# Kernel tuning notes

Measured on AMD Instinct MI355X. Metric: run time of the kernel, lower is better.

The kernel has to match this reference:

```python
import jax, jax.numpy as jnp
import numpy as np

LN_EPS = 1e-5

def _layer_norm(z, w, b):
    m = jnp.mean(z, axis=-1, keepdims=True)
    v = jnp.mean(jnp.square(z - m), axis=-1, keepdims=True)
    return (z - m) * jax.lax.rsqrt(v + LN_EPS) * w + b

def setup_inputs() -> dict:
    key = jax.random.key(0)
    ks = jax.random.split(key, 4)
    B, T, H, L = 32, 512, 1024, 2
    scale = 1.0 / np.sqrt(H)
    x = jax.random.normal(ks[0], (B, T, H), dtype=jnp.float32)
    W = jax.random.normal(ks[1], (L, 4 * H, H), dtype=jnp.float32) * scale
    U = jax.random.normal(ks[2], (L, 4 * H, H), dtype=jnp.float32) * scale
    b = jnp.zeros((L, 4 * H), dtype=jnp.float32)
    lng_w = jnp.ones((L, 4 * H), dtype=jnp.float32)
    lng_b = jnp.zeros((L, 4 * H), dtype=jnp.float32)
    lnc_w = jnp.ones((L, H), dtype=jnp.float32)
    lnc_b = jnp.zeros((L, H), dtype=jnp.float32)
    return {"x": x, "W": W, "b": b, "U": U,
            "lng_w": lng_w, "lng_b": lng_b, "lnc_w": lnc_w, "lnc_b": lnc_b}

def reference(x, W, b, U, lng_w, lng_b, lnc_w, lnc_b):
    # x: (B,T,C). Multi-layer MI-LSTM; dropout=0 (eval). Returns y: (B,T,H).
    L = W.shape[0]
    H = lnc_w.shape[1]
    B = x.shape[0]

    def step(carry, xt):
        hs, cs = carry  # each (L,B,H)
        inp = xt        # (B,C)
        new_h, new_c = [], []
        for l in range(L):
            gx = inp @ W[l].T + b[l]          # (B,4H)
            gh = hs[l] @ U[l].T               # (B,4H)
            gates = gx + gh + gx * gh          # multiplicative integration
            gates = _layer_norm(gates, lng_w[l], lng_b[l])
            i, f, g, o = jnp.split(gates, 4, axis=-1)
            c = jax.nn.sigmoid(f) * cs[l] + jax.nn.sigmoid(i) * jnp.tanh(g)
            c = _layer_norm(c, lnc_w[l], lnc_b[l])
            h = jax.nn.sigmoid(o) * jnp.tanh(c)
            inp = h
            new_h.append(h)
            new_c.append(c)
        return (jnp.stack(new_h), jnp.stack(new_c)), inp

    init = (jnp.zeros((L, B, H), x.dtype), jnp.zeros((L, B, H), x.dtype))
    _, ys = jax.lax.scan(step, init, jnp.swapaxes(x, 0, 1))  # ys: (T,B,H)
    return jnp.swapaxes(ys, 0, 1)
```

## Files before the change

### kernel.cpp

```cpp
#include <hip/hip_runtime.h>


#define TSTEPS 512
#define BATCH  32
#define HDIM   1024
#define GDIM   4096
#define NBLK   256
#define NTHR   256
#define CPB    16
#define KPAD   1032

typedef __attribute__((ext_vector_type(8))) short short8;
typedef __attribute__((ext_vector_type(4))) float f32x4;

#define WLO_OFF   0u
#define HPL_OFF   33554432u
#define G_OFF     37748736u
#define SYNC_OFF  39845888u
#define SMEM_BYTES 152640

#define SW_CENSUS(s)  ((s) * 16)
#define SW_FCNT       128
#define SW_SCNT(s)    (144 + (s) * 16)
#define SW_ROOT       272
#define SW_LCNT(s)    (288 + (s) * 16)

#define AT_RLX __ATOMIC_RELAXED
#define SC_AGT __HIP_MEMORY_SCOPE_AGENT

__device__ __forceinline__ unsigned f2bf(float f) {
  unsigned u = __float_as_uint(f);
  return (u + 0x7FFFu + ((u >> 16) & 1u)) >> 16;
}
__device__ __forceinline__ float sigm(float x) { return 1.f / (1.f + __expf(-x)); }
__device__ __forceinline__ float tanh_(float x) { return 1.f - 2.f / (__expf(2.f * x) + 1.f); }

__device__ __forceinline__ void split8(float4 a, float4 b, short8& hi, short8& lo) {
  float f[8] = {a.x, a.y, a.z, a.w, b.x, b.y, b.z, b.w};
  #pragma unroll
  for (int i = 0; i < 8; ++i) {
    unsigned h = f2bf(f[i]);
    hi[i] = (short)h;
    lo[i] = (short)f2bf(f[i] - __uint_as_float(h << 16));
  }
}

__device__ __forceinline__ int xcc_id() {
  return (int)(__builtin_amdgcn_s_getreg(20 | (3 << 11)) & 7);
}

__device__ __forceinline__ unsigned short* hplane(unsigned char* hbase, int slot, int par, int pl) {
  return (unsigned short*)(hbase + ((unsigned)((slot * 8 + par * 4 + pl)) << 16));
}
__device__ __forceinline__ float* gbase(unsigned char* gb, int l, int par) {
  return (float*)(gb + ((unsigned)(l * 2 + par) << 19));
}

__device__ __forceinline__ void gbar(unsigned* sync, int slot, int n, int nslots, unsigned ep) {
  __syncthreads();
  if (threadIdx.x == 0) {
    unsigned a = __hip_atomic_fetch_add(sync + SW_SCNT(slot), 1u, AT_RLX, SC_AGT);
    if (a == (unsigned)n * ep - 1u)
      __hip_atomic_fetch_add(sync + SW_ROOT, 1u, AT_RLX, SC_AGT);
    while (__hip_atomic_load(sync + SW_ROOT, AT_RLX, SC_AGT) < (unsigned)nslots * ep)
      __builtin_amdgcn_s_sleep(4);
  }
  __syncthreads();
  asm volatile("buffer_inv sc0" ::: "memory");
}

__device__ __forceinline__ void lbar(unsigned* sync, int slot, unsigned target) {
  __syncthreads();
  if (threadIdx.x == 0) {
    __hip_atomic_fetch_add(sync + SW_LCNT(slot), 1u, AT_RLX, SC_AGT);
    while (__hip_atomic_load(sync + SW_LCNT(slot), AT_RLX, SC_AGT) < target)
      __builtin_amdgcn_s_sleep(2);
  }
  __syncthreads();
  asm volatile("buffer_inv sc0" ::: "memory");
}

__device__ __forceinline__ void bred(float& s, float& q, volatile float* red, int tid) {
  #pragma unroll
  for (int o = 32; o > 0; o >>= 1) {
    s += __shfl_xor(s, o, 64);
    q += __shfl_xor(q, o, 64);
  }
  __syncthreads();
  if ((tid & 63) == 0) { int w = tid >> 6; red[w] = s; red[w + 4] = q; }
  __syncthreads();
  s = red[0] + red[1] + red[2] + red[3];
  q = red[4] + red[5] + red[6] + red[7];
  __syncthreads();
}

__device__ __forceinline__ void pointwise2(
    int l, int r, int t, const float* __restrict__ gbuf,
    const float* __restrict__ lngw, const float* __restrict__ lngb,
    const float* __restrict__ lncw, const float* __restrict__ lncb,
    unsigned short* __restrict__ hhi, unsigned short* __restrict__ hlo,
    float* __restrict__ y, float* cst, volatile float* red, int tid)
{
  const float* grow = gbuf + (size_t)r * GDIM;
  const int j0 = tid * 4;
  const float* p0 = grow + j0;
  const float* p1 = grow + 1024 + j0;
  const float* p2 = grow + 2048 + j0;
  const float* p3 = grow + 3072 + j0;
  f32x4 v0, v1, v2, v3;
  asm volatile(
    "global_load_dwordx4 %0, %4, off sc0 sc1\n\t"
    "global_load_dwordx4 %1, %5, off sc0 sc1\n\t"
    "global_load_dwordx4 %2, %6, off sc0 sc1\n\t"
    "global_load_dwordx4 %3, %7, off sc0 sc1\n\t"
    "s_waitcnt vmcnt(0)"
    : "=&v"(v0), "=&v"(v1), "=&v"(v2), "=&v"(v3)
    : "v"(p0), "v"(p1), "v"(p2), "v"(p3)
    : "memory");

  float vals[16];
  #pragma unroll
  for (int k = 0; k < 4; ++k) {
    vals[k]      = v0[k];
    vals[4 + k]  = v1[k];
    vals[8 + k]  = v2[k];
    vals[12 + k] = v3[k];
  }
  float s = 0.f, qq = 0.f;
  #pragma unroll
  for (int i = 0; i < 16; ++i) { s += vals[i]; qq += vals[i] * vals[i]; }
  bred(s, qq, red, tid);
  float m1  = s * (1.f / (float)GDIM);
  float var = qq * (1.f / (float)GDIM) - m1 * m1;
  float inv = rsqrtf(var + 1e-5f);

  float ln[16];
  #pragma unroll
  for (int g = 0; g < 4; ++g) {
    f32x4 gw = *(const f32x4*)(lngw + (size_t)l * GDIM + g * 1024 + j0);
    f32x4 gbv = *(const f32x4*)(lngb + (size_t)l * GDIM + g * 1024 + j0);
    #pragma unroll
    for (int k = 0; k < 4; ++k)
      ln[g * 4 + k] = (vals[g * 4 + k] - m1) * inv * gw[k] + gbv[k];
  }

  f32x4 cold = *(const f32x4*)(cst + j0);
  float cv[4];
  float s2 = 0.f, q2 = 0.f;
  #pragma unroll
  for (int k = 0; k < 4; ++k) {
    float gi = sigm(ln[k]);
    float gf = sigm(ln[4 + k]);
    float gg = tanh_(ln[8 + k]);
    float c  = gf * cold[k] + gi * gg;
    cv[k] = c; s2 += c; q2 += c * c;
  }
  bred(s2, q2, red, tid);
  float m2   = s2 * (1.f / (float)HDIM);
  float vv2  = q2 * (1.f / (float)HDIM) - m2 * m2;
  float inv2 = rsqrtf(vv2 + 1e-5f);

  f32x4 cw = *(const f32x4*)(lncw + (size_t)l * HDIM + j0);
  f32x4 cb = *(const f32x4*)(lncb + (size_t)l * HDIM + j0);
  f32x4 cnew, hv;
  unsigned hhp[4], hlp[4];
  #pragma unroll
  for (int k = 0; k < 4; ++k) {
    float cn = (cv[k] - m2) * inv2 * cw[k] + cb[k];
    cnew[k] = cn;
    float h = sigm(ln[12 + k]) * tanh_(cn);
    hv[k] = h;
    unsigned hh = f2bf(h);
    hhp[k] = hh;
    hlp[k] = f2bf(h - __uint_as_float(hh << 16));
  }
  *(f32x4*)(cst + j0) = cnew;
  uint2 uh, ul;
  uh.x = hhp[0] | (hhp[1] << 16);  uh.y = hhp[2] | (hhp[3] << 16);
  ul.x = hlp[0] | (hlp[1] << 16);  ul.y = hlp[2] | (hlp[3] << 16);
  *(uint2*)(hhi + (size_t)r * HDIM + j0) = uh;
  *(uint2*)(hlo + (size_t)r * HDIM + j0) = ul;
  if (y) *(f32x4*)(y + ((size_t)r * TSTEPS + t) * HDIM + j0) = hv;
}

extern "C" __global__ void __launch_bounds__(NTHR, 1)
milstm_main(const float* __restrict__ x,
            const float* __restrict__ Wm, const float* __restrict__ bv,
            const float* __restrict__ Um,
            const float* __restrict__ lngw, const float* __restrict__ lngb,
            const float* __restrict__ lncw, const float* __restrict__ lncb,
            unsigned char* __restrict__ ws, float* __restrict__ y)
{
  extern __shared__ unsigned char smem[];
  unsigned short* wlds = (unsigned short*)smem;
  float* clds = (float*)(smem + 132096);
  volatile float* red = (volatile float*)(smem + 152576);

  const unsigned short* wlo = (const unsigned short*)(ws + WLO_OFF);
  unsigned char* hbase = ws + HPL_OFF;
  unsigned char* gb    = ws + G_OFF;
  unsigned* sync       = (unsigned*)(ws + SYNC_OFF);

  const int tid = threadIdx.x;
  const int bk  = blockIdx.x;
  const int c0  = bk * CPB;

  #pragma unroll 4
  for (int it = 0; it < 64; ++it) {
    int idx = it * NTHR + tid;
    int mat = idx >> 12;
    int rem = idx & 4095;
    int row = rem >> 8;
    int k4  = rem & 255;
    int l   = mat >> 1;
    const float* src = ((mat & 1) ? Um : Wm) + (size_t)(l * GDIM + c0 + row) * HDIM + k4 * 4;
    float4 f = *(const float4*)src;
    uint2 u;
    u.x = f2bf(f.x) | (f2bf(f.y) << 16);
    u.y = f2bf(f.z) | (f2bf(f.w) << 16);
    *(uint2*)(wlds + (size_t)(mat * CPB + row) * KPAD + k4 * 4) = u;
  }
  for (int i = tid; i < 5 * HDIM; i += NTHR) clds[i] = 0.f;

  __shared__ int sh_slot, sh_rank, sh_n, sh_nslots;
  __syncthreads();
  if (tid == 0) {
    int s = xcc_id();
    sh_slot = s;
    sh_rank = (int)__hip_atomic_fetch_add(sync + SW_CENSUS(s), 1u, AT_RLX, SC_AGT);
    __hip_atomic_fetch_add(sync + SW_FCNT, 1u, AT_RLX, SC_AGT);
    while (__hip_atomic_load(sync + SW_FCNT, AT_RLX, SC_AGT) < (unsigned)NBLK)
      __builtin_amdgcn_s_sleep(4);
    asm volatile("" ::: "memory");
    int ns = 0, nn = 0;
    for (int i = 0; i < 8; ++i) {
      int c = (int)__hip_atomic_load(sync + SW_CENSUS(i), AT_RLX, SC_AGT);
      if (c > 0) ns++;
      if (i == s) nn = c;
    }
    sh_n = nn; sh_nslots = ns;
  }
  __syncthreads();
  const int slot = sh_slot, rank = sh_rank, n = sh_n, nslots = sh_nslots;

  const int lane = tid & 63;
  const int wv   = tid >> 6;
  const int Lw   = wv >> 1;
  const int mt   = wv & 1;
  const int q    = lane >> 4;
  const int r16  = lane & 15;
  const int arow = mt * 16 + r16;

  const unsigned short* bxh = wlds + (size_t)((Lw * 2 + 0) * CPB + r16) * KPAD + q * 8;
  const unsigned short* buh = wlds + (size_t)((Lw * 2 + 1) * CPB + r16) * KPAD + q * 8;
  const unsigned short* bxl = wlo + ((size_t)((Lw * 2 + 0) * GDIM) + c0 + r16) * HDIM + q * 8;
  const unsigned short* bul = wlo + ((size_t)((Lw * 2 + 1) * GDIM) + c0 + r16) * HDIM + q * 8;
  const float bias_v = bv[Lw * GDIM + c0 + r16];

  for (int tk = 0; tk <= TSTEPS; ++tk) {
    const bool act = (Lw == 0) ? (tk < TSTEPS) : (tk >= 1);
    if (act) {
      const unsigned short* p0hi = hplane(hbase, slot, (tk + 1) & 1, 0);
      const unsigned short* p0lo = hplane(hbase, slot, (tk + 1) & 1, 1);
      f32x4 accx = {0.f, 0.f, 0.f, 0.f};
      f32x4 acch = {0.f, 0.f, 0.f, 0.f};
      if (Lw == 0) {
        const float* xp = x + ((size_t)arow * TSTEPS + tk) * HDIM + q * 8;
        const unsigned short* hh = p0hi + arow * HDIM + q * 8;
        const unsigned short* hl = p0lo + arow * HDIM + q * 8;
        short8 wlb[8], ulb[8], hhb[4], hlb[4];
        float4 fab[4], fbb[4];
        #pragma unroll
        for (int i = 0; i < 8; ++i) {
          wlb[i] = *(const short8*)(bxl + i * 32);
          ulb[i] = *(const short8*)(bul + i * 32);
        }
        #pragma unroll
        for (int i = 0; i < 4; ++i) {
          hhb[i] = *(const short8*)(hh + i * 32);
          hlb[i] = *(const short8*)(hl + i * 32);
          fab[i] = *(const float4*)(xp + i * 32);
          fbb[i] = *(const float4*)(xp + i * 32 + 4);
        }
        #pragma unroll
        for (int ch = 0; ch < 32; ++ch) {
          float4 fa = fab[ch & 3], fb = fbb[ch & 3];
          short8 ahh = hhb[ch & 3], ahl = hlb[ch & 3];
          short8 wl = wlb[ch & 7], ul = ulb[ch & 7];
          if (ch + 4 < 32) {
            hhb[ch & 3] = *(const short8*)(hh + (ch + 4) * 32);
            hlb[ch & 3] = *(const short8*)(hl + (ch + 4) * 32);
            fab[ch & 3] = *(const float4*)(xp + (ch + 4) * 32);
            fbb[ch & 3] = *(const float4*)(xp + (ch + 4) * 32 + 4);
          }
          if (ch + 8 < 32) {
            wlb[ch & 7] = *(const short8*)(bxl + (ch + 8) * 32);
            ulb[ch & 7] = *(const short8*)(bul + (ch + 8) * 32);
          }
          short8 axh, axl; split8(fa, fb, axh, axl);
          short8 wh = *(const short8*)(bxh + ch * 32);
          short8 uh = *(const short8*)(buh + ch * 32);
          accx = __builtin_amdgcn_mfma_f32_16x16x32_bf16(axh, wh, accx, 0, 0, 0);
          accx = __builtin_amdgcn_mfma_f32_16x16x32_bf16(axl, wh, accx, 0, 0, 0);
          accx = __builtin_amdgcn_mfma_f32_16x16x32_bf16(axh, wl, accx, 0, 0, 0);
          acch = __builtin_amdgcn_mfma_f32_16x16x32_bf16(ahh, uh, acch, 0, 0, 0);
          acch = __builtin_amdgcn_mfma_f32_16x16x32_bf16(ahl, uh, acch, 0, 0, 0);
          acch = __builtin_amdgcn_mfma_f32_16x16x32_bf16(ahh, ul, acch, 0, 0, 0);
        }
      } else {
        const unsigned short* p1hi = hplane(hbase, slot, tk & 1, 2);
        const unsigned short* p1lo = hplane(hbase, slot, tk & 1, 3);
        const unsigned short* gh_ = p0hi + arow * HDIM + q * 8;
        const unsigned short* gl_ = p0lo + arow * HDIM + q * 8;
        const unsigned short* hh  = p1hi + arow * HDIM + q * 8;
        const unsigned short* hl  = p1lo + arow * HDIM + q * 8;
        short8 wlb[8], ulb[8], axhb[4], axlb[4], ahhb[4], ahlb[4];
        #pragma unroll
        for (int i = 0; i < 8; ++i) {
          wlb[i] = *(const short8*)(bxl + i * 32);
          ulb[i] = *(const short8*)(bul + i * 32);
        }
        #pragma unroll
        for (int i = 0; i < 4; ++i) {
          axhb[i] = *(const short8*)(gh_ + i * 32);
          axlb[i] = *(const short8*)(gl_ + i * 32);
          ahhb[i] = *(const short8*)(hh + i * 32);
          ahlb[i] = *(const short8*)(hl + i * 32);
        }
        #pragma unroll
        for (int ch = 0; ch < 32; ++ch) {
          short8 axh = axhb[ch & 3], axl = axlb[ch & 3];
          short8 ahh = ahhb[ch & 3], ahl = ahlb[ch & 3];
          short8 wl = wlb[ch & 7], ul = ulb[ch & 7];
          if (ch + 4 < 32) {
            axhb[ch & 3] = *(const short8*)(gh_ + (ch + 4) * 32);
            axlb[ch & 3] = *(const short8*)(gl_ + (ch + 4) * 32);
            ahhb[ch & 3] = *(const short8*)(hh + (ch + 4) * 32);
            ahlb[ch & 3] = *(const short8*)(hl + (ch + 4) * 32);
          }
          if (ch + 8 < 32) {
            wlb[ch & 7] = *(const short8*)(bxl + (ch + 8) * 32);
            ulb[ch & 7] = *(const short8*)(bul + (ch + 8) * 32);
          }
          short8 wh = *(const short8*)(bxh + ch * 32);
          short8 uh = *(const short8*)(buh + ch * 32);
          accx = __builtin_amdgcn_mfma_f32_16x16x32_bf16(axh, wh, accx, 0, 0, 0);
          accx = __builtin_amdgcn_mfma_f32_16x16x32_bf16(axl, wh, accx, 0, 0, 0);
          accx = __builtin_amdgcn_mfma_f32_16x16x32_bf16(axh, wl, accx, 0, 0, 0);
          acch = __builtin_amdgcn_mfma_f32_16x16x32_bf16(ahh, uh, acch, 0, 0, 0);
          acch = __builtin_amdgcn_mfma_f32_16x16x32_bf16(ahl, uh, acch, 0, 0, 0);
          acch = __builtin_amdgcn_mfma_f32_16x16x32_bf16(ahh, ul, acch, 0, 0, 0);
        }
      }
      float* gbuf = (Lw == 0) ? gbase(gb, 0, tk & 1) : gbase(gb, 1, (tk - 1) & 1);
      #pragma unroll
      for (int rg = 0; rg < 4; ++rg) {
        float gx = accx[rg] + bias_v;
        float gh = acch[rg];
        int row = mt * 16 + q * 4 + rg;
        __hip_atomic_store(&gbuf[row * GDIM + c0 + r16], gx + gh + gx * gh, AT_RLX, SC_AGT);
      }
    }
    gbar(sync, slot, n, nslots, (unsigned)(tk + 1));

    for (int task = rank; task < 64; task += n) {
      int o = (task - rank) / n;
      if (o >= 5) break;
      int l = task >> 5, r = task & 31;
      float* cst = clds + o * HDIM;
      if (l == 0) {
        if (tk < TSTEPS)
          pointwise2(0, r, tk, gbase(gb, 0, tk & 1), lngw, lngb, lncw, lncb,
                     hplane(hbase, slot, tk & 1, 0), hplane(hbase, slot, tk & 1, 1),
                     (float*)0, cst, red, tid);
      } else {
        if (tk >= 1)
          pointwise2(1, r, tk - 1, gbase(gb, 1, (tk - 1) & 1), lngw, lngb, lncw, lncb,
                     hplane(hbase, slot, (tk - 1) & 1, 2), hplane(hbase, slot, (tk - 1) & 1, 3),
                     y, cst, red, tid);
      }
    }
    lbar(sync, slot, (unsigned)n * (unsigned)(tk + 1));
  }
}

extern "C" __global__ void __launch_bounds__(256)
milstm_prep_wlo(const float* __restrict__ Wm, const float* __restrict__ Um,
                unsigned short* __restrict__ wlo)
{
  int v = blockIdx.x * 256 + threadIdx.x;
  int mat = v >> 20;
  int rem = v & 1048575;
  int col = rem >> 8;
  int k4  = rem & 255;
  const float* src = ((mat & 1) ? Um : Wm) + (size_t)((mat >> 1) * GDIM + col) * HDIM + k4 * 4;
  float4 f = *(const float4*)src;
  float fv[4] = {f.x, f.y, f.z, f.w};
  unsigned lo[4];
  #pragma unroll
  for (int i = 0; i < 4; ++i) {
    unsigned h = f2bf(fv[i]);
    lo[i] = f2bf(fv[i] - __uint_as_float(h << 16));
  }
  uint2 u;
  u.x = lo[0] | (lo[1] << 16);
  u.y = lo[2] | (lo[3] << 16);
  *(uint2*)(wlo + ((size_t)mat * GDIM + col) * HDIM + k4 * 4) = u;
}

extern "C" __global__ void __launch_bounds__(256)
milstm_prep_init(unsigned* __restrict__ hz, unsigned* __restrict__ sync)
{
  int v = blockIdx.x * 256 + threadIdx.x;
  if (v < 1048576) hz[v] = 0u;
  else if (v < 1048576 + 1024) sync[v - 1048576] = 0u;
}

extern "C" void kernel_launch(void* const* d_in, const int* in_sizes, int n_in,
                              void* d_out, int out_size, void* d_ws, size_t ws_size,
                              hipStream_t stream)
{
  const float* x    = (const float*)d_in[0];
  const float* Wm   = (const float*)d_in[1];
  const float* bv   = (const float*)d_in[2];
  const float* Um   = (const float*)d_in[3];
  const float* lngw = (const float*)d_in[4];
  const float* lngb = (const float*)d_in[5];
  const float* lncw = (const float*)d_in[6];
  const float* lncb = (const float*)d_in[7];
  float* y = (float*)d_out;

  unsigned char* ws = (unsigned char*)d_ws;
  unsigned short* wlo = (unsigned short*)(ws + WLO_OFF);
  unsigned* hz   = (unsigned*)(ws + HPL_OFF);
  unsigned* sync = (unsigned*)(ws + SYNC_OFF);

  hipLaunchKernelGGL(milstm_prep_wlo, dim3(16384), dim3(256), 0, stream, Wm, Um, wlo);
  hipLaunchKernelGGL(milstm_prep_init, dim3(4101), dim3(256), 0, stream, hz, sync);
  (void)hipFuncSetAttribute((const void*)milstm_main,
                            hipFuncAttributeMaxDynamicSharedMemorySize, SMEM_BYTES);
  hipLaunchKernelGGL(milstm_main, dim3(NBLK), dim3(NTHR), SMEM_BYTES, stream,
                     x, Wm, bv, Um, lngw, lngb, lncw, lncb, ws, y);
}
```

Measured before the change: 18.61 ms.

## Quantize low-part weight residuals to int8 with per-row scales

```diff
diff --git a/kernel.cpp b/kernel.cpp
--- a/kernel.cpp
+++ b/kernel.cpp
@@ -13,7 +13,8 @@
 typedef __attribute__((ext_vector_type(8))) short short8;
 typedef __attribute__((ext_vector_type(4))) float f32x4;
 
-#define WLO_OFF   0u
+#define WQ8_OFF   0u
+#define WSC_OFF   16777216u
 #define HPL_OFF   33554432u
 #define G_OFF     37748736u
 #define SYNC_OFF  39845888u
@@ -43,6 +44,20 @@
     hi[i] = (short)h;
     lo[i] = (short)f2bf(f[i] - __uint_as_float(h << 16));
   }
+}
+
+__device__ __forceinline__ short8 expand_q8(uint2 v) {
+  short8 r;
+  #pragma unroll
+  for (int j = 0; j < 2; ++j) {
+    unsigned u = j ? v.y : v.x;
+    #pragma unroll
+    for (int b = 0; b < 4; ++b) {
+      float f = (float)((u >> (8 * b)) & 0xffu) - 128.f;
+      r[j * 4 + b] = (short)(__float_as_uint(f) >> 16);
+    }
+  }
+  return r;
 }
 
 __device__ __forceinline__ int xcc_id() {
@@ -196,7 +211,8 @@
   float* clds = (float*)(smem + 132096);
   volatile float* red = (volatile float*)(smem + 152576);
 
-  const unsigned short* wlo = (const unsigned short*)(ws + WLO_OFF);
+  const unsigned char* wq8 = (const unsigned char*)(ws + WQ8_OFF);
+  const float* wsc = (const float*)(ws + WSC_OFF);
   unsigned char* hbase = ws + HPL_OFF;
   unsigned char* gb    = ws + G_OFF;
   unsigned* sync       = (unsigned*)(ws + SYNC_OFF);
@@ -253,8 +269,10 @@
 
   const unsigned short* bxh = wlds + (size_t)((Lw * 2 + 0) * CPB + r16) * KPAD + q * 8;
   const unsigned short* buh = wlds + (size_t)((Lw * 2 + 1) * CPB + r16) * KPAD + q * 8;
-  const unsigned short* bxl = wlo + ((size_t)((Lw * 2 + 0) * GDIM) + c0 + r16) * HDIM + q * 8;
-  const unsigned short* bul = wlo + ((size_t)((Lw * 2 + 1) * GDIM) + c0 + r16) * HDIM + q * 8;
+  const unsigned char* bxq = wq8 + ((size_t)((Lw * 2 + 0) * GDIM) + c0 + r16) * HDIM + q * 8;
+  const unsigned char* buq = wq8 + ((size_t)((Lw * 2 + 1) * GDIM) + c0 + r16) * HDIM + q * 8;
+  const float sw = wsc[(Lw * 2 + 0) * GDIM + c0 + r16];
+  const float su = wsc[(Lw * 2 + 1) * GDIM + c0 + r16];
   const float bias_v = bv[Lw * GDIM + c0 + r16];
 
   for (int tk = 0; tk <= TSTEPS; ++tk) {
@@ -262,50 +280,50 @@
     if (act) {
       const unsigned short* p0hi = hplane(hbase, slot, (tk + 1) & 1, 0);
       const unsigned short* p0lo = hplane(hbase, slot, (tk + 1) & 1, 1);
-      f32x4 accx = {0.f, 0.f, 0.f, 0.f};
-      f32x4 acch = {0.f, 0.f, 0.f, 0.f};
+      f32x4 accx  = {0.f, 0.f, 0.f, 0.f};
+      f32x4 acch  = {0.f, 0.f, 0.f, 0.f};
+      f32x4 accqx = {0.f, 0.f, 0.f, 0.f};
+      f32x4 accqh = {0.f, 0.f, 0.f, 0.f};
       if (Lw == 0) {
         const float* xp = x + ((size_t)arow * TSTEPS + tk) * HDIM + q * 8;
         const unsigned short* hh = p0hi + arow * HDIM + q * 8;
         const unsigned short* hl = p0lo + arow * HDIM + q * 8;
-        short8 wlb[8], ulb[8], hhb[4], hlb[4];
+        short8 hhb[4], hlb[4];
         float4 fab[4], fbb[4];
-        #pragma unroll
-        for (int i = 0; i < 8; ++i) {
-          wlb[i] = *(const short8*)(bxl + i * 32);
-          ulb[i] = *(const short8*)(bul + i * 32);
-        }
+        uint2 wqb[4], uqb[4];
         #pragma unroll
         for (int i = 0; i < 4; ++i) {
           hhb[i] = *(const short8*)(hh + i * 32);
           hlb[i] = *(const short8*)(hl + i * 32);
           fab[i] = *(const float4*)(xp + i * 32);
           fbb[i] = *(const float4*)(xp + i * 32 + 4);
+          wqb[i] = *(const uint2*)(bxq + i * 32);
+          uqb[i] = *(const uint2*)(buq + i * 32);
         }
-        #pragma unroll
+        #pragma unroll 4
         for (int ch = 0; ch < 32; ++ch) {
           float4 fa = fab[ch & 3], fb = fbb[ch & 3];
           short8 ahh = hhb[ch & 3], ahl = hlb[ch & 3];
-          short8 wl = wlb[ch & 7], ul = ulb[ch & 7];
+          uint2 wq = wqb[ch & 3], uq = uqb[ch & 3];
           if (ch + 4 < 32) {
             hhb[ch & 3] = *(const short8*)(hh + (ch + 4) * 32);
             hlb[ch & 3] = *(const short8*)(hl + (ch + 4) * 32);
             fab[ch & 3] = *(const float4*)(xp + (ch + 4) * 32);
             fbb[ch & 3] = *(const float4*)(xp + (ch + 4) * 32 + 4);
-          }
-          if (ch + 8 < 32) {
-            wlb[ch & 7] = *(const short8*)(bxl + (ch + 8) * 32);
-            ulb[ch & 7] = *(const short8*)(bul + (ch + 8) * 32);
+            wqb[ch & 3] = *(const uint2*)(bxq + (ch + 4) * 32);
+            uqb[ch & 3] = *(const uint2*)(buq + (ch + 4) * 32);
           }
           short8 axh, axl; split8(fa, fb, axh, axl);
+          short8 wl = expand_q8(wq);
+          short8 ul = expand_q8(uq);
           short8 wh = *(const short8*)(bxh + ch * 32);
           short8 uh = *(const short8*)(buh + ch * 32);
-          accx = __builtin_amdgcn_mfma_f32_16x16x32_bf16(axh, wh, accx, 0, 0, 0);
-          accx = __builtin_amdgcn_mfma_f32_16x16x32_bf16(axl, wh, accx, 0, 0, 0);
-          accx = __builtin_amdgcn_mfma_f32_16x16x32_bf16(axh, wl, accx, 0, 0, 0);
-          acch = __builtin_amdgcn_mfma_f32_16x16x32_bf16(ahh, uh, acch, 0, 0, 0);
-          acch = __builtin_amdgcn_mfma_f32_16x16x32_bf16(ahl, uh, acch, 0, 0, 0);
-          acch = __builtin_amdgcn_mfma_f32_16x16x32_bf16(ahh, ul, acch, 0, 0, 0);
+          accx  = __builtin_amdgcn_mfma_f32_16x16x32_bf16(axh, wh, accx, 0, 0, 0);
+          accx  = __builtin_amdgcn_mfma_f32_16x16x32_bf16(axl, wh, accx, 0, 0, 0);
+          accqx = __builtin_amdgcn_mfma_f32_16x16x32_bf16(axh, wl, accqx, 0, 0, 0);
+          acch  = __builtin_amdgcn_mfma_f32_16x16x32_bf16(ahh, uh, acch, 0, 0, 0);
+          acch  = __builtin_amdgcn_mfma_f32_16x16x32_bf16(ahl, uh, acch, 0, 0, 0);
+          accqh = __builtin_amdgcn_mfma_f32_16x16x32_bf16(ahh, ul, accqh, 0, 0, 0);
         }
       } else {
         const unsigned short* p1hi = hplane(hbase, slot, tk & 1, 2);
@@ -314,49 +332,47 @@
         const unsigned short* gl_ = p0lo + arow * HDIM + q * 8;
         const unsigned short* hh  = p1hi + arow * HDIM + q * 8;
         const unsigned short* hl  = p1lo + arow * HDIM + q * 8;
-        short8 wlb[8], ulb[8], axhb[4], axlb[4], ahhb[4], ahlb[4];
-        #pragma unroll
-        for (int i = 0; i < 8; ++i) {
-          wlb[i] = *(const short8*)(bxl + i * 32);
-          ulb[i] = *(const short8*)(bul + i * 32);
-        }
+        short8 axhb[4], axlb[4], ahhb[4], ahlb[4];
+        uint2 wqb[4], uqb[4];
         #pragma unroll
         for (int i = 0; i < 4; ++i) {
           axhb[i] = *(const short8*)(gh_ + i * 32);
           axlb[i] = *(const short8*)(gl_ + i * 32);
           ahhb[i] = *(const short8*)(hh + i * 32);
           ahlb[i] = *(const short8*)(hl + i * 32);
+          wqb[i] = *(const uint2*)(bxq + i * 32);
+          uqb[i] = *(const uint2*)(buq + i * 32);
         }
-        #pragma unroll
+        #pragma unroll 4
         for (int ch = 0; ch < 32; ++ch) {
           short8 axh = axhb[ch & 3], axl = axlb[ch & 3];
           short8 ahh = ahhb[ch & 3], ahl = ahlb[ch & 3];
-          short8 wl = wlb[ch & 7], ul = ulb[ch & 7];
+          uint2 wq = wqb[ch & 3], uq = uqb[ch & 3];
           if (ch + 4 < 32) {
             axhb[ch & 3] = *(const short8*)(gh_ + (ch + 4) * 32);
             axlb[ch & 3] = *(const short8*)(gl_ + (ch + 4) * 32);
             ahhb[ch & 3] = *(const short8*)(hh + (ch + 4) * 32);
             ahlb[ch & 3] = *(const short8*)(hl + (ch + 4) * 32);
+            wqb[ch & 3] = *(const uint2*)(bxq + (ch + 4) * 32);
+            uqb[ch & 3] = *(const uint2*)(buq + (ch + 4) * 32);
           }
-          if (ch + 8 < 32) {
-            wlb[ch & 7] = *(const short8*)(bxl + (ch + 8) * 32);
-            ulb[ch & 7] = *(const short8*)(bul + (ch + 8) * 32);
-          }
+          short8 wl = expand_q8(wq);
+          short8 ul = expand_q8(uq);
           short8 wh = *(const short8*)(bxh + ch * 32);
           short8 uh = *(const short8*)(buh + ch * 32);
-          accx = __builtin_amdgcn_mfma_f32_16x16x32_bf16(axh, wh, accx, 0, 0, 0);
-          accx = __builtin_amdgcn_mfma_f32_16x16x32_bf16(axl, wh, accx, 0, 0, 0);
-          accx = __builtin_amdgcn_mfma_f32_16x16x32_bf16(axh, wl, accx, 0, 0, 0);
-          acch = __builtin_amdgcn_mfma_f32_16x16x32_bf16(ahh, uh, acch, 0, 0, 0);
-          acch = __builtin_amdgcn_mfma_f32_16x16x32_bf16(ahl, uh, acch, 0, 0, 0);
-          acch = __builtin_amdgcn_mfma_f32_16x16x32_bf16(ahh, ul, acch, 0, 0, 0);
+          accx  = __builtin_amdgcn_mfma_f32_16x16x32_bf16(axh, wh, accx, 0, 0, 0);
+          accx  = __builtin_amdgcn_mfma_f32_16x16x32_bf16(axl, wh, accx, 0, 0, 0);
+          accqx = __builtin_amdgcn_mfma_f32_16x16x32_bf16(axh, wl, accqx, 0, 0, 0);
+          acch  = __builtin_amdgcn_mfma_f32_16x16x32_bf16(ahh, uh, acch, 0, 0, 0);
+          acch  = __builtin_amdgcn_mfma_f32_16x16x32_bf16(ahl, uh, acch, 0, 0, 0);
+          accqh = __builtin_amdgcn_mfma_f32_16x16x32_bf16(ahh, ul, accqh, 0, 0, 0);
         }
       }
       float* gbuf = (Lw == 0) ? gbase(gb, 0, tk & 1) : gbase(gb, 1, (tk - 1) & 1);
       #pragma unroll
       for (int rg = 0; rg < 4; ++rg) {
-        float gx = accx[rg] + bias_v;
-        float gh = acch[rg];
+        float gx = accx[rg] + sw * accqx[rg] + bias_v;
+        float gh = acch[rg] + su * accqh[rg];
         int row = mt * 16 + q * 4 + rg;
         __hip_atomic_store(&gbuf[row * GDIM + c0 + r16], gx + gh + gx * gh, AT_RLX, SC_AGT);
       }
@@ -384,28 +400,48 @@
   }
 }
 
-extern "C" __global__ void __launch_bounds__(256)
-milstm_prep_wlo(const float* __restrict__ Wm, const float* __restrict__ Um,
-                unsigned short* __restrict__ wlo)
+extern "C" __global__ void __launch_bounds__(64)
+milstm_prep_wq8(const float* __restrict__ Wm, const float* __restrict__ Um,
+                unsigned char* __restrict__ wq8, float* __restrict__ wsc)
 {
-  int v = blockIdx.x * 256 + threadIdx.x;
-  int mat = v >> 20;
-  int rem = v & 1048575;
-  int col = rem >> 8;
-  int k4  = rem & 255;
-  const float* src = ((mat & 1) ? Um : Wm) + (size_t)((mat >> 1) * GDIM + col) * HDIM + k4 * 4;
-  float4 f = *(const float4*)src;
-  float fv[4] = {f.x, f.y, f.z, f.w};
-  unsigned lo[4];
+  int b = blockIdx.x;
+  int mat = b >> 12;
+  int col = b & 4095;
+  int lane = threadIdx.x;
+  const float* src = ((mat & 1) ? Um : Wm)
+                   + ((size_t)((mat >> 1) * GDIM + col)) * HDIM + lane * 16;
+  float lo[16];
+  float m = 0.f;
   #pragma unroll
   for (int i = 0; i < 4; ++i) {
-    unsigned h = f2bf(fv[i]);
-    lo[i] = f2bf(fv[i] - __uint_as_float(h << 16));
-  }
-  uint2 u;
-  u.x = lo[0] | (lo[1] << 16);
-  u.y = lo[2] | (lo[3] << 16);
-  *(uint2*)(wlo + ((size_t)mat * GDIM + col) * HDIM + k4 * 4) = u;
+    float4 f = *(const float4*)(src + i * 4);
+    float w4[4] = {f.x, f.y, f.z, f.w};
+    #pragma unroll
+    for (int j = 0; j < 4; ++j) {
+      unsigned hb = f2bf(w4[j]);
+      float l_ = w4[j] - __uint_as_float(hb << 16);
+      lo[i * 4 + j] = l_;
+      m = fmaxf(m, fabsf(l_));
+    }
+  }
+  #pragma unroll
+  for (int o = 32; o > 0; o >>= 1) m = fmaxf(m, __shfl_xor(m, o, 64));
+  float s = (m > 0.f) ? (m * (1.f / 127.f)) : 1.f;
+  float rs = 1.f / s;
+  unsigned bytes[16];
+  #pragma unroll
+  for (int i = 0; i < 16; ++i) {
+    float qf = rintf(lo[i] * rs);
+    qf = fminf(fmaxf(qf, -127.f), 127.f);
+    bytes[i] = (unsigned)(int)(qf + 128.f);
+  }
+  uint4 u;
+  u.x = bytes[0]  | (bytes[1]  << 8) | (bytes[2]  << 16) | (bytes[3]  << 24);
+  u.y = bytes[4]  | (bytes[5]  << 8) | (bytes[6]  << 16) | (bytes[7]  << 24);
+  u.z = bytes[8]  | (bytes[9]  << 8) | (bytes[10] << 16) | (bytes[11] << 24);
+  u.w = bytes[12] | (bytes[13] << 8) | (bytes[14] << 16) | (bytes[15] << 24);
+  *(uint4*)(wq8 + ((size_t)mat * GDIM + col) * HDIM + lane * 16) = u;
+  if (lane == 0) wsc[mat * GDIM + col] = s;
 }
 
 extern "C" __global__ void __launch_bounds__(256)
@@ -431,11 +467,12 @@
   float* y = (float*)d_out;
 
   unsigned char* ws = (unsigned char*)d_ws;
-  unsigned short* wlo = (unsigned short*)(ws + WLO_OFF);
+  unsigned char* wq8 = ws + WQ8_OFF;
+  float* wsc = (float*)(ws + WSC_OFF);
   unsigned* hz   = (unsigned*)(ws + HPL_OFF);
   unsigned* sync = (unsigned*)(ws + SYNC_OFF);
 
-  hipLaunchKernelGGL(milstm_prep_wlo, dim3(16384), dim3(256), 0, stream, Wm, Um, wlo);
+  hipLaunchKernelGGL(milstm_prep_wq8, dim3(16384), dim3(64), 0, stream, Wm, Um, wq8, wsc);
   hipLaunchKernelGGL(milstm_prep_init, dim3(4101), dim3(256), 0, stream, hz, sync);
   (void)hipFuncSetAttribute((const void*)milstm_main,
                             hipFuncAttributeMaxDynamicSharedMemorySize, SMEM_BYTES);
```

Result: faster. 17.02 ms (-8.6%).
